# Performance work log

Measured on AMD Instinct MI355X. Metric: run time of the kernel, lower is better.

Reference implementation:

```python
import jax, jax.numpy as jnp
import numpy as np

N = 50000      # nodes
E = 800000     # edges (before self loops)
H = 4          # heads
C = 32         # hidden_channels per head
HC = H * C     # 128
L = 3          # num_layers - 2 conv blocks
G = 128        # graphs in batch
OUT = 10       # out_channels
VOCAB = 100
EPS = 1e-5


def setup_inputs() -> dict:
    key = jax.random.key(0)
    ks = jax.random.split(key, 16)
    s = 0.1
    return {
        "x_idx": jax.random.randint(ks[0], (N,), 0, VOCAB),
        "edge_index": jax.random.randint(ks[1], (2, E), 0, N),
        "batch": jnp.sort(jax.random.randint(ks[2], (N,), 0, G)),
        "embed": jax.random.normal(ks[3], (VOCAB, HC), jnp.float32) * s,
        "bn_gamma": jnp.ones((L, HC), jnp.float32),
        "bn_beta": jnp.zeros((L, HC), jnp.float32),
        "lin_W": jax.random.normal(ks[4], (L, C, HC), jnp.float32) * s,   # maps HC -> C (hidden)
        "lin_b": jnp.zeros((L, C), jnp.float32),
        "gat_W": jax.random.normal(ks[5], (L, HC, C), jnp.float32) * s,   # maps C -> H*C
        "att_src": jax.random.normal(ks[6], (L, H, C), jnp.float32) * s,
        "att_dst": jax.random.normal(ks[7], (L, H, C), jnp.float32) * s,
        "gat_b": jnp.zeros((L, HC), jnp.float32),
        "readout_W": jax.random.normal(ks[8], (OUT, HC), jnp.float32) * s,
        "readout_b": jnp.zeros((OUT,), jnp.float32),
    }


def _segment_softmax(logits, seg, num_segments):
    # logits: [E, H], seg: [E]
    m = jax.ops.segment_max(logits, seg, num_segments=num_segments)
    m = jnp.where(jnp.isfinite(m), m, 0.0)
    e = jnp.exp(logits - m[seg])
    z = jax.ops.segment_sum(e, seg, num_segments=num_segments)
    return e / (z[seg] + 1e-16)


def _forward(x_idx, edge_index, batch, embed, bn_gamma, bn_beta, lin_W, lin_b,
             gat_W, att_src, att_dst, gat_b, readout_W, readout_b):
    x = embed[x_idx]                                   # [N, HC]
    loops = jnp.arange(N)
    src = jnp.concatenate([edge_index[0], loops])      # add_self_loops=True
    dst = jnp.concatenate([edge_index[1], loops])
    for l in range(L):
        # BatchNorm1d (batch statistics)
        mean = jnp.mean(x, axis=0)
        var = jnp.var(x, axis=0)
        x = bn_gamma[l] * (x - mean) * jax.lax.rsqrt(var + EPS) + bn_beta[l]
        # Linear(HC -> C) + relu; dropout = identity (eval)
        x = jax.nn.relu(x @ lin_W[l].T + lin_b[l])      # [N, C]
        # GATConv(C -> C, heads=H, concat)
        h = (x @ gat_W[l].T).reshape(N, H, C)           # [N, H, C]
        a_src = jnp.sum(h * att_src[l], axis=-1)        # [N, H]
        a_dst = jnp.sum(h * att_dst[l], axis=-1)        # [N, H]
        logits = jax.nn.leaky_relu(a_src[src] + a_dst[dst], 0.2)  # [E+N, H]
        alpha = _segment_softmax(logits, dst, N)        # softmax over in-edges of each dst
        msg = h[src] * alpha[:, :, None]                # [E+N, H, C]
        x = jax.ops.segment_sum(msg, dst, num_segments=N).reshape(N, HC) + gat_b[l]
    x = x @ readout_W.T + readout_b                     # [N, OUT]
    return jax.ops.segment_sum(x, batch, num_segments=G)  # [G, OUT]


def reference(x_idx, edge_index, batch, embed, bn_gamma, bn_beta, lin_W, lin_b,
              gat_W, att_src, att_dst, gat_b, readout_W, readout_b):
    return _forward(x_idx, edge_index, batch, embed, bn_gamma, bn_beta, lin_W, lin_b,
                    gat_W, att_src, att_dst, gat_b, readout_W, readout_b)
```

## Files before the change

### kernel.cpp

```cpp
#include <hip/hip_runtime.h>

constexpr int NN   = 50000;
constexpr int NE   = 800000;
constexpr int NHD  = 4;
constexpr int CC   = 32;
constexpr int HCC  = 128;
constexpr int NL   = 3;
constexpr int NG   = 128;
constexpr int NOUT = 10;
constexpr float BN_EPS = 1e-5f;

constexpr int X2S = 67;
constexpr int YS = 33;
constexpr int NSLOT = 64;
constexpr int NBUK = (NN + 127) / 128;
constexpr int EB  = 8192;

__device__ inline unsigned f2bf_pack(float a, float b) {
    unsigned ua = __float_as_uint(a); ua += 0x7FFFu + ((ua >> 16) & 1u);
    unsigned ub = __float_as_uint(b); ub += 0x7FFFu + ((ub >> 16) & 1u);
    return (ua >> 16) | (ub & 0xFFFF0000u);
}
__device__ inline float bf_lo(unsigned p) { return __uint_as_float(p << 16); }
__device__ inline float bf_hi(unsigned p) { return __uint_as_float(p & 0xFFFF0000u); }

__global__ __launch_bounds__(256) void k_embed_stats(const int* __restrict__ idx,
                                                     const float* __restrict__ embed,
                                                     float* __restrict__ x,
                                                     float* __restrict__ stats) {
    int tid = threadIdx.x;
    int i0 = blockIdx.x * 256 + tid;
    int stride = gridDim.x * 256;
    float s = 0.f, q = 0.f;
    for (int i = i0; i < NN * HCC; i += stride) {
        float v = embed[idx[i >> 7] * HCC + (i & 127)];
        x[i] = v; s += v; q += v * v;
    }
    __shared__ float ssum[256], ssq[256];
    ssum[tid] = s; ssq[tid] = q;
    __syncthreads();
    int slot = blockIdx.x & (NSLOT - 1);
    if (tid < HCC) {
        atomicAdd(&stats[slot * 256 + tid],       ssum[tid] + ssum[tid + HCC]);
        atomicAdd(&stats[slot * 256 + HCC + tid], ssq[tid]  + ssq[tid + HCC]);
    }
}

__global__ __launch_bounds__(256) void k_bhist(const int* __restrict__ ei,
                                               int* __restrict__ bkcnt) {
    __shared__ int hist[NBUK];
    int b = blockIdx.x, t = threadIdx.x;
    int e0 = b * EB, nE = min(EB, NE - e0);
    for (int i = t; i < NBUK; i += 256) hist[i] = 0;
    __syncthreads();
    for (int i = t; i < nE; i += 256)
        atomicAdd(&hist[ei[NE + e0 + i] >> 7], 1);
    __syncthreads();
    for (int i = t; i < NBUK; i += 256)
        if (hist[i]) atomicAdd(&bkcnt[i], hist[i]);
}

__global__ __launch_bounds__(512) void k_bscan(const int* __restrict__ bkcnt,
                                               int* __restrict__ bbase,
                                               int* __restrict__ bcnt,
                                               int* __restrict__ rowptr) {
    __shared__ int sc[512];
    int t = threadIdx.x;
    int v = (t < NBUK) ? bkcnt[t] : 0;
    sc[t] = v;
    __syncthreads();
#pragma unroll
    for (int off = 1; off < 512; off <<= 1) {
        int u = (t >= off) ? sc[t - off] : 0;
        __syncthreads();
        sc[t] += u;
        __syncthreads();
    }
    if (t < NBUK) {
        int excl = sc[t] - v;
        bbase[t] = excl;
        bcnt[t]  = excl;
    }
    if (t == 0) rowptr[NN] = NE;
}

__global__ __launch_bounds__(256) void k_bin(const int* __restrict__ ei,
                                             int* __restrict__ bcnt,
                                             unsigned* __restrict__ e_src) {
    __shared__ int hist[NBUK], base[NBUK];
    int b = blockIdx.x, t = threadIdx.x;
    int e0 = b * EB;
    int nE = min(EB, NE - e0);

    for (int i = t; i < NBUK; i += 256) hist[i] = 0;
    __syncthreads();
    for (int i = t; i < nE; i += 256)
        atomicAdd(&hist[ei[NE + e0 + i] >> 7], 1);
    __syncthreads();
    for (int i = t; i < NBUK; i += 256) {
        int c = hist[i];
        if (c) base[i] = atomicAdd(&bcnt[i], c);
        hist[i] = 0;
    }
    __syncthreads();
    for (int i = t; i < nE; i += 256) {
        int e = e0 + i;
        int d = ei[NE + e];
        int s = ei[e];
        int bk = d >> 7;
        int pos = base[bk] + atomicAdd(&hist[bk], 1);
        e_src[pos] = (unsigned)s | ((unsigned)(d & 127) << 17);
    }
}

__global__ __launch_bounds__(256) void k_place(const int* __restrict__ bbase,
                                               unsigned* __restrict__ e_src,
                                               int* __restrict__ rowptr) {
    __shared__ int lcnt[128], sc[128], lrp[128], cnt[128];
    int b = blockIdx.x, t = threadIdx.x;
    int d0 = b * 128;
    int rS = bbase[b];
    int rE = (b + 1 < NBUK) ? bbase[b + 1] : NE;
    int n = rE - rS;
    if (t < 128) { lcnt[t] = 0; cnt[t] = 0; }
    __syncthreads();
    unsigned pk[14];
#pragma unroll
    for (int k = 0; k < 14; k++) {
        int i = t + k * 256;
        if (i < n) {
            pk[k] = e_src[rS + i];
            atomicAdd(&lcnt[pk[k] >> 17], 1);
        }
    }
    __syncthreads();
    if (t < 128) sc[t] = lcnt[t];
    __syncthreads();
#pragma unroll
    for (int off = 1; off < 128; off <<= 1) {
        int u = (t < 128 && t >= off) ? sc[t - off] : 0;
        __syncthreads();
        if (t < 128) sc[t] += u;
        __syncthreads();
    }
    if (t < 128) {
        int start = rS + sc[t] - lcnt[t];
        lrp[t] = start;
        int d = d0 + t;
        if (d < NN) rowptr[d] = start;
    }
    __syncthreads();
#pragma unroll
    for (int k = 0; k < 14; k++) {
        int i = t + k * 256;
        if (i < n) {
            unsigned p = pk[k];
            int dl = p >> 17;
            int pos = lrp[dl] + atomicAdd(&cnt[dl], 1);
            e_src[pos] = p & 0x1FFFFu;
        }
    }
}

__global__ __launch_bounds__(256) void k_fused(const float* __restrict__ x,
                                               const float* __restrict__ stats,
                                               const float* __restrict__ gamma,
                                               const float* __restrict__ beta,
                                               const float* __restrict__ W1,
                                               const float* __restrict__ b1,
                                               const float* __restrict__ W2,
                                               const float* __restrict__ aS,
                                               const float* __restrict__ aD,
                                               unsigned* __restrict__ h,
                                               float* __restrict__ asrc,
                                               float* __restrict__ adst) {
    __shared__ unsigned xb2[64 * X2S];
    __shared__ float yt[64 * YS];
    __shared__ float ssl[256];
    int tid = threadIdx.x;
    int node0 = blockIdx.x * 64;
    int nNodes = min(64, NN - node0);

    if (tid < 128) {
        float s = 0.f, q = 0.f;
        for (int sl = 0; sl < NSLOT; sl++) {
            s += stats[sl * 256 + tid];
            q += stats[sl * 256 + HCC + tid];
        }
        float mean = s * (1.0f / NN);
        float var  = q * (1.0f / NN) - mean * mean;
        float sc   = gamma[tid] * rsqrtf(var + BN_EPS);
        ssl[tid]       = sc;
        ssl[HCC + tid] = beta[tid] - mean * sc;
    }
    __syncthreads();

    {
        int cS = (tid * 4) & 127;
        float4 scv = *(const float4*)&ssl[cS];
        float4 shv = *(const float4*)&ssl[HCC + cS];
        for (int f4 = tid; f4 < nNodes * 32; f4 += 256) {
            int f = f4 * 4; int n = f >> 7; int c = f & 127;
            float4 xv = *(const float4*)(x + (size_t)(node0 + n) * HCC + c);
            float v0 = xv.x * scv.x + shv.x;
            float v1 = xv.y * scv.y + shv.y;
            float v2 = xv.z * scv.z + shv.z;
            float v3 = xv.w * scv.w + shv.w;
            unsigned* dst = &xb2[n * X2S + (c >> 1)];
            dst[0] = f2bf_pack(v0, v1);
            dst[1] = f2bf_pack(v2, v3);
        }
    }
    __syncthreads();

    int lane = tid & 63;
    int wv = __builtin_amdgcn_readfirstlane(tid >> 6);
    int n = lane;

    {
        int j0 = wv * 8;
        const float* w1p = W1 + j0 * 128;
        float acc[8];
#pragma unroll
        for (int k = 0; k < 8; k++) acc[k] = b1[j0 + k];
        if (n < nNodes) {
            for (int cb = 0; cb < 128; cb += 4) {
                unsigned p0 = xb2[n * X2S + (cb >> 1)];
                unsigned p1 = xb2[n * X2S + (cb >> 1) + 1];
                float xv0 = bf_lo(p0), xv1 = bf_hi(p0);
                float xv2 = bf_lo(p1), xv3 = bf_hi(p1);
#pragma unroll
                for (int k = 0; k < 8; k++) {
                    float4 w = *(const float4*)&w1p[k * 128 + cb];
                    acc[k] += xv0 * w.x + xv1 * w.y + xv2 * w.z + xv3 * w.w;
                }
            }
#pragma unroll
            for (int k = 0; k < 8; k++) yt[n * YS + j0 + k] = fmaxf(acc[k], 0.f);
        }
    }
    __syncthreads();

    if (n < nNodes) {
        int k0 = wv * 32, hd = wv;
        const float* w2p = W2 + k0 * 32;
        const float* aSp = aS + hd * 32;
        const float* aDp = aD + hd * 32;
        float yreg[32];
#pragma unroll
        for (int j = 0; j < 32; j++) yreg[j] = yt[n * YS + j];
        float sa = 0.f, da = 0.f;
        unsigned* hrow = h + (size_t)(node0 + n) * 64;
        for (int kb = 0; kb < 32; kb += 8) {
            float acck[8];
#pragma unroll
            for (int kk = 0; kk < 8; kk++) acck[kk] = 0.f;
#pragma unroll
            for (int j = 0; j < 32; j += 4) {
#pragma unroll
                for (int kk = 0; kk < 8; kk++) {
                    float4 w = *(const float4*)&w2p[(kb + kk) * 32 + j];
                    acck[kk] += yreg[j] * w.x + yreg[j + 1] * w.y +
                                yreg[j + 2] * w.z + yreg[j + 3] * w.w;
                }
            }
#pragma unroll
            for (int kk = 0; kk < 8; kk++) {
                sa += acck[kk] * aSp[kb + kk];
                da += acck[kk] * aDp[kb + kk];
            }
            uint4 pk;
            pk.x = f2bf_pack(acck[0], acck[1]);
            pk.y = f2bf_pack(acck[2], acck[3]);
            pk.z = f2bf_pack(acck[4], acck[5]);
            pk.w = f2bf_pack(acck[6], acck[7]);
            *(uint4*)(hrow + ((kb) >> 1) + (k0 >> 1)) = pk;
        }
        asrc[(node0 + n) * 4 + hd] = sa;
        adst[(node0 + n) * 4 + hd] = da;
    }
}

__global__ __launch_bounds__(256) void k_agg(const int* __restrict__ rowptr,
                                             const int* __restrict__ e_src,
                                             const float* __restrict__ asrc,
                                             const float* __restrict__ adst,
                                             const unsigned* __restrict__ h,
                                             const float* __restrict__ gat_b,
                                             float* __restrict__ xo,
                                             float* __restrict__ stats,
                                             int do_stats) {
    int tid = threadIdx.x, lane = tid & 63, wv = tid >> 6;
    int g  = lane >> 4;
    int li = lane & 15;
    int hd = li >> 2;
    int d  = blockIdx.x * 16 + wv * 4 + g;

    float4 bA = *(const float4*)(gat_b + li * 8);
    float4 bB = *(const float4*)(gat_b + li * 8 + 4);

    int begin = rowptr[d];
    int end   = rowptr[d + 1];
    float adv = adst[d * 4 + hd];
    float asl = asrc[d * 4 + hd];
    uint4 hs  = *(const uint4*)(h + (size_t)d * 64 + li * 4);

    float acc[8];
#pragma unroll
    for (int k = 0; k < 8; k++) acc[k] = 0.f;
    float ws = 0.f;

    int s[4];
    if (begin < end) {
#pragma unroll
        for (int t = 0; t < 4; t++) s[t] = e_src[min(begin + t, end - 1)];
    }

    for (int j = begin; j < end; j += 4) {
        uint4 hv[4];
#pragma unroll
        for (int t = 0; t < 4; t++) hv[t] = *(const uint4*)(h + (size_t)s[t] * 64 + li * 4);
        float av[4];
#pragma unroll
        for (int t = 0; t < 4; t++) av[t] = asrc[s[t] * 4 + hd];
        int jn = j + 4;
        int sn[4];
#pragma unroll
        for (int t = 0; t < 4; t++) sn[t] = s[t];
        if (jn < end) {
#pragma unroll
            for (int t = 0; t < 4; t++) sn[t] = e_src[min(jn + t, end - 1)];
        }
        float w[4];
#pragma unroll
        for (int t = 0; t < 4; t++) {
            float l = av[t] + adv; l = l > 0.f ? l : 0.2f * l;
            w[t] = (j + t < end) ? __expf(l) : 0.f;
        }
#pragma unroll
        for (int t = 0; t < 4; t++) {
            acc[0] += w[t] * bf_lo(hv[t].x); acc[1] += w[t] * bf_hi(hv[t].x);
            acc[2] += w[t] * bf_lo(hv[t].y); acc[3] += w[t] * bf_hi(hv[t].y);
            acc[4] += w[t] * bf_lo(hv[t].z); acc[5] += w[t] * bf_hi(hv[t].z);
            acc[6] += w[t] * bf_lo(hv[t].w); acc[7] += w[t] * bf_hi(hv[t].w);
            ws += w[t];
        }
#pragma unroll
        for (int t = 0; t < 4; t++) s[t] = sn[t];
    }

    {
        float l = asl + adv; l = l > 0.f ? l : 0.2f * l;
        float w = __expf(l);
        acc[0] += w * bf_lo(hs.x); acc[1] += w * bf_hi(hs.x);
        acc[2] += w * bf_lo(hs.y); acc[3] += w * bf_hi(hs.y);
        acc[4] += w * bf_lo(hs.z); acc[5] += w * bf_hi(hs.z);
        acc[6] += w * bf_lo(hs.w); acc[7] += w * bf_hi(hs.w);
        ws += w;
    }

    float inv = 1.0f / (ws + 1e-16f);
    float o[8];
    o[0] = acc[0] * inv + bA.x; o[1] = acc[1] * inv + bA.y;
    o[2] = acc[2] * inv + bA.z; o[3] = acc[3] * inv + bA.w;
    o[4] = acc[4] * inv + bB.x; o[5] = acc[5] * inv + bB.y;
    o[6] = acc[6] * inv + bB.z; o[7] = acc[7] * inv + bB.w;
    float* orow = xo + (size_t)d * HCC + li * 8;
    *(float4*)orow       = make_float4(o[0], o[1], o[2], o[3]);
    *(float4*)(orow + 4) = make_float4(o[4], o[5], o[6], o[7]);

    if (!do_stats) return;
    __shared__ float redS[16 * 128], redQ[16 * 128];
    int r = wv * 4 + g;
#pragma unroll
    for (int k = 0; k < 8; k++) {
        redS[r * 128 + li * 8 + k] = o[k];
        redQ[r * 128 + li * 8 + k] = o[k] * o[k];
    }
    __syncthreads();
    int slot = blockIdx.x & (NSLOT - 1);
    if (tid < 128) {
        float v = 0.f;
#pragma unroll
        for (int rr = 0; rr < 16; rr++) v += redS[rr * 128 + tid];
        atomicAdd(&stats[slot * 256 + tid], v);
    } else {
        int c = tid - 128;
        float v = 0.f;
#pragma unroll
        for (int rr = 0; rr < 16; rr++) v += redQ[rr * 128 + c];
        atomicAdd(&stats[slot * 256 + HCC + c], v);
    }
}

__global__ __launch_bounds__(256) void k_pool(const float* __restrict__ x,
                                              const int* __restrict__ batch,
                                              float* __restrict__ gsum,
                                              float* __restrict__ gcnt) {
    int nb = blockIdx.x * 64, t = threadIdx.x;
    int c = t & 127, half = t >> 7;
    float s = 0.f, cnt = 0.f;
    int curg = -1;
    for (int k = half; k < 64; k += 2) {
        int n = nb + k;
        if (n >= NN) break;
        int g = batch[n];
        if (g != curg) {
            if (curg >= 0) {
                atomicAdd(&gsum[curg * HCC + c], s);
                if (c == 0) atomicAdd(&gcnt[curg], cnt);
            }
            curg = g; s = 0.f; cnt = 0.f;
        }
        s += x[(size_t)n * HCC + c];
        cnt += 1.f;
    }
    if (curg >= 0) {
        atomicAdd(&gsum[curg * HCC + c], s);
        if (c == 0) atomicAdd(&gcnt[curg], cnt);
    }
}

__global__ __launch_bounds__(128) void k_out(const float* __restrict__ gsum,
                                             const float* __restrict__ gcnt,
                                             const float* __restrict__ W,
                                             const float* __restrict__ bb,
                                             float* __restrict__ out) {
    __shared__ float v[128];
    int g = blockIdx.x, t = threadIdx.x;
    v[t] = gsum[g * HCC + t];
    __syncthreads();
    if (t < NOUT) {
        float acc = gcnt[g] * bb[t];
        const float* wr = W + t * HCC;
        for (int c = 0; c < HCC; c++) acc += v[c] * wr[c];
        out[g * NOUT + t] = acc;
    }
}

extern "C" void kernel_launch(void* const* d_in, const int* in_sizes, int n_in,
                              void* d_out, int out_size, void* d_ws, size_t ws_size,
                              hipStream_t stream) {
    const int*   x_idx = (const int*)d_in[0];
    const int*   ei    = (const int*)d_in[1];
    const int*   batch = (const int*)d_in[2];
    const float* embed = (const float*)d_in[3];
    const float* bn_g  = (const float*)d_in[4];
    const float* bn_b  = (const float*)d_in[5];
    const float* lin_W = (const float*)d_in[6];
    const float* lin_b = (const float*)d_in[7];
    const float* gat_W = (const float*)d_in[8];
    const float* att_s = (const float*)d_in[9];
    const float* att_d = (const float*)d_in[10];
    const float* gat_b = (const float*)d_in[11];
    const float* ro_W  = (const float*)d_in[12];
    const float* ro_b  = (const float*)d_in[13];
    float* out = (float*)d_out;

    const size_t STG = (size_t)NSLOT * 256;
    float*    x     = (float*)d_ws;
    unsigned* h     = (unsigned*)(x + (size_t)NN * HCC);
    float*    asrc  = (float*)(h + (size_t)NN * 64);
    float*    adst  = asrc + (size_t)NN * NHD;
    float*    stats = adst + (size_t)NN * NHD;
    float*    gsum  = stats + 3 * STG;
    float*    gcnt  = gsum + (size_t)NG * HCC;
    int*      bkcnt  = (int*)(gcnt + NG);
    int*      bbase  = bkcnt + NBUK;
    int*      bcnt   = bbase + NBUK;
    int*      rowptr = bcnt + NBUK;
    unsigned* e_src  = (unsigned*)(rowptr + NN + 1);

    hipMemsetAsync(stats, 0,
                   (3 * STG + (size_t)NG * HCC + NG) * sizeof(float) + NBUK * sizeof(int),
                   stream);

    k_embed_stats<<<512, 256, 0, stream>>>(x_idx, embed, x, stats);
    k_bhist<<<(NE + EB - 1) / EB, 256, 0, stream>>>(ei, bkcnt);
    k_bscan<<<1, 512, 0, stream>>>(bkcnt, bbase, bcnt, rowptr);
    k_bin<<<(NE + EB - 1) / EB, 256, 0, stream>>>(ei, bcnt, e_src);
    k_place<<<NBUK, 256, 0, stream>>>(bbase, e_src, rowptr);

    for (int l = 0; l < NL; ++l) {
        k_fused<<<(NN + 63) / 64, 256, 0, stream>>>(x, stats + l * STG,
                                                    bn_g + l * HCC, bn_b + l * HCC,
                                                    lin_W + l * CC * HCC, lin_b + l * CC,
                                                    gat_W + l * HCC * CC,
                                                    att_s + l * NHD * CC,
                                                    att_d + l * NHD * CC,
                                                    h, asrc, adst);
        k_agg<<<NN / 16, 256, 0, stream>>>(rowptr, (const int*)e_src, asrc, adst, h,
                                           gat_b + l * HCC, x,
                                           stats + (l + 1) * STG,
                                           (l < NL - 1) ? 1 : 0);
    }

    k_pool<<<(NN + 63) / 64, 256, 0, stream>>>(x, batch, gsum, gcnt);
    k_out<<<NG, 128, 0, stream>>>(gsum, gcnt, ro_W, ro_b, out);
}
```

Before: 373.4 us.

## Store activations as bf16 and fuse graph pooling into final aggregation

The node feature buffer between layers is now stored as packed bf16 instead of fp32, which halves the write traffic in aggregation and the read traffic in the fused linear kernel. The final layer's aggregation now accumulates per-graph sums directly with block-local reduction and atomics, so the separate pooling kernel and its full read of x are gone. Graph node counts are computed in the histogram kernel. BN statistics are still computed from fp32 values, so normalization uses slightly different inputs than the stored bf16 values.

```diff
diff --git a/kernel.cpp b/kernel.cpp
--- a/kernel.cpp
+++ b/kernel.cpp
@@ -26,38 +26,59 @@
 
 __global__ __launch_bounds__(256) void k_embed_stats(const int* __restrict__ idx,
                                                      const float* __restrict__ embed,
-                                                     float* __restrict__ x,
+                                                     unsigned* __restrict__ xp,
                                                      float* __restrict__ stats) {
     int tid = threadIdx.x;
     int i0 = blockIdx.x * 256 + tid;
     int stride = gridDim.x * 256;
-    float s = 0.f, q = 0.f;
-    for (int i = i0; i < NN * HCC; i += stride) {
-        float v = embed[idx[i >> 7] * HCC + (i & 127)];
-        x[i] = v; s += v; q += v * v;
-    }
-    __shared__ float ssum[256], ssq[256];
-    ssum[tid] = s; ssq[tid] = q;
+    float s0 = 0.f, s1 = 0.f, q0 = 0.f, q1 = 0.f;
+    for (int i = i0; i < NN * 64; i += stride) {
+        int n = i >> 6, c2 = (i & 63) << 1;
+        float2 ev = *(const float2*)(embed + (size_t)idx[n] * HCC + c2);
+        xp[i] = f2bf_pack(ev.x, ev.y);
+        s0 += ev.x; q0 += ev.x * ev.x;
+        s1 += ev.y; q1 += ev.y * ev.y;
+    }
+    __shared__ float A[256], B[256], C[256], D[256];
+    A[tid] = s0; B[tid] = s1; C[tid] = q0; D[tid] = q1;
     __syncthreads();
     int slot = blockIdx.x & (NSLOT - 1);
-    if (tid < HCC) {
-        atomicAdd(&stats[slot * 256 + tid],       ssum[tid] + ssum[tid + HCC]);
-        atomicAdd(&stats[slot * 256 + HCC + tid], ssq[tid]  + ssq[tid + HCC]);
+    if (tid < 64) {
+        int p = tid;
+        float S0 = A[p] + A[p + 64] + A[p + 128] + A[p + 192];
+        float S1 = B[p] + B[p + 64] + B[p + 128] + B[p + 192];
+        float Q0 = C[p] + C[p + 64] + C[p + 128] + C[p + 192];
+        float Q1 = D[p] + D[p + 64] + D[p + 128] + D[p + 192];
+        atomicAdd(&stats[slot * 256 + 2 * p],           S0);
+        atomicAdd(&stats[slot * 256 + 2 * p + 1],       S1);
+        atomicAdd(&stats[slot * 256 + HCC + 2 * p],     Q0);
+        atomicAdd(&stats[slot * 256 + HCC + 2 * p + 1], Q1);
     }
 }
 
 __global__ __launch_bounds__(256) void k_bhist(const int* __restrict__ ei,
-                                               int* __restrict__ bkcnt) {
+                                               int* __restrict__ bkcnt,
+                                               const int* __restrict__ batch,
+                                               float* __restrict__ gcnt) {
     __shared__ int hist[NBUK];
+    __shared__ int lgc[NG];
     int b = blockIdx.x, t = threadIdx.x;
     int e0 = b * EB, nE = min(EB, NE - e0);
     for (int i = t; i < NBUK; i += 256) hist[i] = 0;
+    for (int i = t; i < NG; i += 256) lgc[i] = 0;
     __syncthreads();
     for (int i = t; i < nE; i += 256)
         atomicAdd(&hist[ei[NE + e0 + i] >> 7], 1);
+    int n0 = b * 512;
+    for (int i = t; i < 512; i += 256) {
+        int n = n0 + i;
+        if (n < NN) atomicAdd(&lgc[batch[n]], 1);
+    }
     __syncthreads();
     for (int i = t; i < NBUK; i += 256)
         if (hist[i]) atomicAdd(&bkcnt[i], hist[i]);
+    for (int i = t; i < NG; i += 256)
+        if (lgc[i]) atomicAdd(&gcnt[i], (float)lgc[i]);
 }
 
 __global__ __launch_bounds__(512) void k_bscan(const int* __restrict__ bkcnt,
@@ -162,7 +183,7 @@
     }
 }
 
-__global__ __launch_bounds__(256) void k_fused(const float* __restrict__ x,
+__global__ __launch_bounds__(256) void k_fused(const unsigned* __restrict__ xp,
                                                const float* __restrict__ stats,
                                                const float* __restrict__ gamma,
                                                const float* __restrict__ beta,
@@ -176,7 +197,7 @@
                                                float* __restrict__ adst) {
     __shared__ unsigned xb2[64 * X2S];
     __shared__ float yt[64 * YS];
-    __shared__ float ssl[256];
+    __shared__ float __attribute__((aligned(16))) ssl[256];
     int tid = threadIdx.x;
     int node0 = blockIdx.x * 64;
     int nNodes = min(64, NN - node0);
@@ -196,19 +217,19 @@
     __syncthreads();
 
     {
-        int cS = (tid * 4) & 127;
-        float4 scv = *(const float4*)&ssl[cS];
-        float4 shv = *(const float4*)&ssl[HCC + cS];
-        for (int f4 = tid; f4 < nNodes * 32; f4 += 256) {
-            int f = f4 * 4; int n = f >> 7; int c = f & 127;
-            float4 xv = *(const float4*)(x + (size_t)(node0 + n) * HCC + c);
-            float v0 = xv.x * scv.x + shv.x;
-            float v1 = xv.y * scv.y + shv.y;
-            float v2 = xv.z * scv.z + shv.z;
-            float v3 = xv.w * scv.w + shv.w;
-            unsigned* dst = &xb2[n * X2S + (c >> 1)];
-            dst[0] = f2bf_pack(v0, v1);
-            dst[1] = f2bf_pack(v2, v3);
+        for (int q4 = tid; q4 < nNodes * 16; q4 += 256) {
+            int n = q4 >> 4, c8 = q4 & 15;
+            uint4 xv = *(const uint4*)(xp + (size_t)(node0 + n) * 64 + c8 * 4);
+            int c = c8 * 8;
+            float4 sc0 = *(const float4*)&ssl[c];
+            float4 sc1 = *(const float4*)&ssl[c + 4];
+            float4 sh0 = *(const float4*)&ssl[HCC + c];
+            float4 sh1 = *(const float4*)&ssl[HCC + c + 4];
+            unsigned* dst = &xb2[n * X2S + c8 * 4];
+            dst[0] = f2bf_pack(bf_lo(xv.x) * sc0.x + sh0.x, bf_hi(xv.x) * sc0.y + sh0.y);
+            dst[1] = f2bf_pack(bf_lo(xv.y) * sc0.z + sh0.z, bf_hi(xv.y) * sc0.w + sh0.w);
+            dst[2] = f2bf_pack(bf_lo(xv.z) * sc1.x + sh1.x, bf_hi(xv.z) * sc1.y + sh1.y);
+            dst[3] = f2bf_pack(bf_lo(xv.w) * sc1.z + sh1.z, bf_hi(xv.w) * sc1.w + sh1.w);
         }
     }
     __syncthreads();
@@ -287,9 +308,11 @@
                                              const float* __restrict__ adst,
                                              const unsigned* __restrict__ h,
                                              const float* __restrict__ gat_b,
-                                             float* __restrict__ xo,
+                                             unsigned* __restrict__ xo,
                                              float* __restrict__ stats,
-                                             int do_stats) {
+                                             const int* __restrict__ batch,
+                                             float* __restrict__ gsum,
+                                             int mode) {
     int tid = threadIdx.x, lane = tid & 63, wv = tid >> 6;
     int g  = lane >> 4;
     int li = lane & 15;
@@ -365,59 +388,57 @@
     o[2] = acc[2] * inv + bA.z; o[3] = acc[3] * inv + bA.w;
     o[4] = acc[4] * inv + bB.x; o[5] = acc[5] * inv + bB.y;
     o[6] = acc[6] * inv + bB.z; o[7] = acc[7] * inv + bB.w;
-    float* orow = xo + (size_t)d * HCC + li * 8;
-    *(float4*)orow       = make_float4(o[0], o[1], o[2], o[3]);
-    *(float4*)(orow + 4) = make_float4(o[4], o[5], o[6], o[7]);
-
-    if (!do_stats) return;
+
     __shared__ float redS[16 * 128], redQ[16 * 128];
+    __shared__ int bg[16];
     int r = wv * 4 + g;
-#pragma unroll
-    for (int k = 0; k < 8; k++) {
-        redS[r * 128 + li * 8 + k] = o[k];
-        redQ[r * 128 + li * 8 + k] = o[k] * o[k];
-    }
-    __syncthreads();
-    int slot = blockIdx.x & (NSLOT - 1);
-    if (tid < 128) {
-        float v = 0.f;
-#pragma unroll
-        for (int rr = 0; rr < 16; rr++) v += redS[rr * 128 + tid];
-        atomicAdd(&stats[slot * 256 + tid], v);
+
+    if (mode == 1) {
+        uint4 pk;
+        pk.x = f2bf_pack(o[0], o[1]);
+        pk.y = f2bf_pack(o[2], o[3]);
+        pk.z = f2bf_pack(o[4], o[5]);
+        pk.w = f2bf_pack(o[6], o[7]);
+        *(uint4*)(xo + (size_t)d * 64 + li * 4) = pk;
+
+#pragma unroll
+        for (int k = 0; k < 8; k++) {
+            redS[r * 128 + li * 8 + k] = o[k];
+            redQ[r * 128 + li * 8 + k] = o[k] * o[k];
+        }
+        __syncthreads();
+        int slot = blockIdx.x & (NSLOT - 1);
+        if (tid < 128) {
+            float v = 0.f;
+#pragma unroll
+            for (int rr = 0; rr < 16; rr++) v += redS[rr * 128 + tid];
+            atomicAdd(&stats[slot * 256 + tid], v);
+        } else {
+            int c = tid - 128;
+            float v = 0.f;
+#pragma unroll
+            for (int rr = 0; rr < 16; rr++) v += redQ[rr * 128 + c];
+            atomicAdd(&stats[slot * 256 + HCC + c], v);
+        }
     } else {
-        int c = tid - 128;
-        float v = 0.f;
-#pragma unroll
-        for (int rr = 0; rr < 16; rr++) v += redQ[rr * 128 + c];
-        atomicAdd(&stats[slot * 256 + HCC + c], v);
-    }
-}
-
-__global__ __launch_bounds__(256) void k_pool(const float* __restrict__ x,
-                                              const int* __restrict__ batch,
-                                              float* __restrict__ gsum,
-                                              float* __restrict__ gcnt) {
-    int nb = blockIdx.x * 64, t = threadIdx.x;
-    int c = t & 127, half = t >> 7;
-    float s = 0.f, cnt = 0.f;
-    int curg = -1;
-    for (int k = half; k < 64; k += 2) {
-        int n = nb + k;
-        if (n >= NN) break;
-        int g = batch[n];
-        if (g != curg) {
-            if (curg >= 0) {
-                atomicAdd(&gsum[curg * HCC + c], s);
-                if (c == 0) atomicAdd(&gcnt[curg], cnt);
+        if (li == 0) bg[r] = batch[d];
+#pragma unroll
+        for (int k = 0; k < 8; k++) redS[r * 128 + li * 8 + k] = o[k];
+        __syncthreads();
+        if (tid < 128) {
+            float sacc = 0.f;
+            int curg = bg[0];
+#pragma unroll
+            for (int rr = 0; rr < 16; rr++) {
+                int gg = bg[rr];
+                if (gg != curg) {
+                    atomicAdd(&gsum[curg * HCC + tid], sacc);
+                    sacc = 0.f; curg = gg;
+                }
+                sacc += redS[rr * 128 + tid];
             }
-            curg = g; s = 0.f; cnt = 0.f;
-        }
-        s += x[(size_t)n * HCC + c];
-        cnt += 1.f;
-    }
-    if (curg >= 0) {
-        atomicAdd(&gsum[curg * HCC + c], s);
-        if (c == 0) atomicAdd(&gcnt[curg], cnt);
+            atomicAdd(&gsum[curg * HCC + tid], sacc);
+        }
     }
 }
 
@@ -458,8 +479,8 @@
     float* out = (float*)d_out;
 
     const size_t STG = (size_t)NSLOT * 256;
-    float*    x     = (float*)d_ws;
-    unsigned* h     = (unsigned*)(x + (size_t)NN * HCC);
+    unsigned* xp    = (unsigned*)d_ws;
+    unsigned* h     = xp + (size_t)NN * 64;
     float*    asrc  = (float*)(h + (size_t)NN * 64);
     float*    adst  = asrc + (size_t)NN * NHD;
     float*    stats = adst + (size_t)NN * NHD;
@@ -475,14 +496,14 @@
                    (3 * STG + (size_t)NG * HCC + NG) * sizeof(float) + NBUK * sizeof(int),
                    stream);
 
-    k_embed_stats<<<512, 256, 0, stream>>>(x_idx, embed, x, stats);
-    k_bhist<<<(NE + EB - 1) / EB, 256, 0, stream>>>(ei, bkcnt);
+    k_embed_stats<<<512, 256, 0, stream>>>(x_idx, embed, xp, stats);
+    k_bhist<<<(NE + EB - 1) / EB, 256, 0, stream>>>(ei, bkcnt, batch, gcnt);
     k_bscan<<<1, 512, 0, stream>>>(bkcnt, bbase, bcnt, rowptr);
     k_bin<<<(NE + EB - 1) / EB, 256, 0, stream>>>(ei, bcnt, e_src);
     k_place<<<NBUK, 256, 0, stream>>>(bbase, e_src, rowptr);
 
     for (int l = 0; l < NL; ++l) {
-        k_fused<<<(NN + 63) / 64, 256, 0, stream>>>(x, stats + l * STG,
+        k_fused<<<(NN + 63) / 64, 256, 0, stream>>>(xp, stats + l * STG,
                                                     bn_g + l * HCC, bn_b + l * HCC,
                                                     lin_W + l * CC * HCC, lin_b + l * CC,
                                                     gat_W + l * HCC * CC,
@@ -490,11 +511,11 @@
                                                     att_d + l * NHD * CC,
                                                     h, asrc, adst);
         k_agg<<<NN / 16, 256, 0, stream>>>(rowptr, (const int*)e_src, asrc, adst, h,
-                                           gat_b + l * HCC, x,
+                                           gat_b + l * HCC, xp,
                                            stats + (l + 1) * STG,
-                                           (l < NL - 1) ? 1 : 0);
-    }
-
-    k_pool<<<(NN + 63) / 64, 256, 0, stream>>>(x, batch, gsum, gcnt);
+                                           batch, gsum,
+                                           (l < NL - 1) ? 1 : 2);
+    }
+
     k_out<<<NG, 128, 0, stream>>>(gsum, gcnt, ro_W, ro_b, out);
 }
```

Measured after the change: 341.4 us. 8.6% less time.
